# Kernel optimization log

Measured on AMD Instinct MI355X. Metric: run time of the kernel, lower is better.

## Reference

```python
import jax, jax.numpy as jnp
import numpy as np

N = 50000   # total nodes (50 graphs x 1000 nodes)
E = 800000  # edges (avg degree 16)
H = 128     # hidden_dim == input_dim
B = 50      # number of graphs
L = 3       # n_GNN_layers
NEG = 0.2   # LeakyReLU slope
EPS = 1e-5  # BatchNorm eps


def _lrelu(v):
    return jnp.where(v >= 0, v, NEG * v)


def setup_inputs() -> dict:
    key = jax.random.key(0)
    ks = jax.random.split(key, 16)
    s = 0.05
    inp = {
        "x": jax.random.normal(ks[0], (N, H), jnp.float32),
        "edge_index": jax.random.randint(ks[1], (2, E), 0, N, dtype=jnp.int64),
        "edge_attr": jax.random.uniform(ks[2], (E,), jnp.float32),
        "batch": jnp.sort(jax.random.randint(ks[3], (N,), 0, B, dtype=jnp.int64)),
        # per-layer GCN params (3 identical-shape layers stacked on axis 0)
        "Wg": (jax.random.normal(ks[4], (L, H, H)) * s).astype(jnp.float32),   # GCNConv.lin (no bias)
        "bg": jnp.zeros((L, H), jnp.float32),                                  # GCNConv.bias
        "We": (jax.random.normal(ks[5], (L, 2 * H, H)) * s).astype(jnp.float32),  # edge_lin
        "be": jnp.zeros((L, H), jnp.float32),
        "Wl": (jax.random.normal(ks[6], (L, H, H)) * s).astype(jnp.float32),   # post-conv Linear
        "bl": jnp.zeros((L, H), jnp.float32),
        "gamma": jnp.ones((L, H), jnp.float32),                                # BatchNorm affine
        "beta": jnp.zeros((L, H), jnp.float32),
        # final MLP head
        "Wf1": (jax.random.normal(ks[7], (H, H)) * s).astype(jnp.float32),
        "bf1": jnp.zeros((H,), jnp.float32),
        "Wf2": (jax.random.normal(ks[8], (H, H // 2)) * s).astype(jnp.float32),
        "bf2": jnp.zeros((H // 2,), jnp.float32),
        "Wf3": (jax.random.normal(ks[9], (H // 2, 2)) * s).astype(jnp.float32),
        "bf3": jnp.zeros((2,), jnp.float32),
    }
    return inp


def reference(x, edge_index, edge_attr, batch, Wg, bg, We, be, Wl, bl, gamma, beta,
              Wf1, bf1, Wf2, bf2, Wf3, bf3):
    n = x.shape[0]
    # edge_attr = |edge_attr| is used only for gcn_norm's edge weights, which the
    # 'node_concate' message ignores; self-loops from gcn_norm DO affect messages.
    _ = jnp.abs(edge_attr)
    loop = jnp.arange(n, dtype=edge_index.dtype)
    row = jnp.concatenate([edge_index[0], loop])  # source j
    col = jnp.concatenate([edge_index[1], loop])  # target i

    z = x
    for l in range(L):
        h = z @ Wg[l]                                           # GCNConv.lin (bias=False)
        msg = jnp.concatenate([h[col], h[row]], axis=1) @ We[l] + be[l]  # edge_lin(cat[x_i, x_j])
        agg = jax.ops.segment_sum(msg, col, num_segments=n) + bg[l]      # scatter-add + conv bias
        h2 = _lrelu(agg @ Wl[l] + bl[l])                        # Linear + LeakyReLU(0.2)
        mu = h2.mean(axis=0)
        var = h2.var(axis=0)                                    # biased var (BatchNorm training)
        z = gamma[l] * (h2 - mu) * jax.lax.rsqrt(var + EPS) + beta[l]

    # global_mean_pool over graph segments
    sums = jax.ops.segment_sum(z, batch, num_segments=B)
    cnt = jax.ops.segment_sum(jnp.ones((n, 1), z.dtype), batch, num_segments=B)
    pooled = sums / jnp.maximum(cnt, 1.0)

    h = _lrelu(pooled @ Wf1 + bf1)
    h = _lrelu(h @ Wf2 + bf2)
    return h @ Wf3 + bf3
```

## Files before the change

### kernel.cpp

```cpp
#include <hip/hip_runtime.h>
#include <hip/hip_fp16.h>

#define H 128
#define NEG 0.2f
#define EPSBN 1e-5f
#define BM 32

__device__ __forceinline__ float lrelu(float v){ return v >= 0.f ? v : NEG*v; }

union HU { __half2 h; unsigned int u; };

typedef __attribute__((ext_vector_type(8))) short bf16x8;
typedef __attribute__((ext_vector_type(4))) float f32x4;
#define MFMA16(a,b,c) __builtin_amdgcn_mfma_f32_16x16x32_bf16(a,b,c,0,0,0)

__device__ __forceinline__ unsigned short bf16_rn(float x){
  unsigned int u = __float_as_uint(x);
  u += 0x7fffu + ((u >> 16) & 1u);
  return (unsigned short)(u >> 16);
}
__device__ __forceinline__ float bf16f(unsigned short h){
  return __uint_as_float(((unsigned int)h) << 16);
}

__device__ __forceinline__ void asplit(const float* As, int aofs, bf16x8& ah, bf16x8& al){
  float av[8];
  *reinterpret_cast<float4*>(&av[0]) = *reinterpret_cast<const float4*>(&As[aofs]);
  *reinterpret_cast<float4*>(&av[4]) = *reinterpret_cast<const float4*>(&As[aofs+4]);
  #pragma unroll
  for (int j=0;j<8;j++){
    unsigned short h = bf16_rn(av[j]);
    ah[j] = (short)h;
    al[j] = (short)bf16_rn(av[j] - bf16f(h));
  }
}

__global__ void prep1_kernel(const float* __restrict__ We, const float* __restrict__ Wl,
                             float* __restrict__ Ntmp){
  int l = blockIdx.x >> 7;
  int k = blockIdx.x & 127;
  int j = threadIdx.x;
  __shared__ float WeS[2*H];
  if (j < H) WeS[j] = We[(size_t)(l*2*H + k)*H + j];
  else       WeS[j] = We[(size_t)(l*2*H + 128 + k)*H + (j-128)];
  __syncthreads();
  const float* wl = Wl + (size_t)l*H*H;
  int sel = (j >> 7) << 7;
  int jj = j & 127;
  float acc = 0.f;
  #pragma unroll 8
  for (int m=0;m<H;m++) acc += WeS[sel + m] * wl[m*H + jj];
  Ntmp[(size_t)(l*H + k)*256 + j] = acc;
}

__global__ void prep2_kernel(const float* __restrict__ Wg, const float* __restrict__ Ntmp,
                             float* __restrict__ Mcomb){
  int l = blockIdx.x >> 7;
  int k = blockIdx.x & 127;
  int j = threadIdx.x;
  __shared__ float WgS[H];
  if (j < H) WgS[j] = Wg[(size_t)(l*H + k)*H + j];
  __syncthreads();
  const float* nt = Ntmp + (size_t)l*H*256;
  float acc = 0.f;
  #pragma unroll 8
  for (int m=0;m<H;m++) acc += WgS[m] * nt[m*256 + j];
  Mcomb[(size_t)(l*H + k)*256 + j] = acc;
}

__global__ void prep3_kernel(const float* __restrict__ Mcomb,
                             unsigned short* __restrict__ Mfh, unsigned short* __restrict__ Mfl){
  int bid = blockIdx.x;
  int l  = bid >> 6;
  int ks = (bid >> 4) & 3;
  int ct = bid & 15;
  int lane = threadIdx.x;
  const float* M = Mcomb + (size_t)l*H*256;
  size_t base = ((((size_t)l*4 + ks)*16 + ct)*64 + lane)*8;
  int col = ct*16 + (lane & 15);
  int g = lane >> 4;
  #pragma unroll
  for (int j=0;j<8;j++){
    int k = ks*32 + 8*g + j;
    float v = M[(size_t)k*256 + col];
    unsigned short hi = bf16_rn(v);
    unsigned short lo = bf16_rn(v - bf16f(hi));
    Mfh[base + j] = hi;
    Mfl[base + j] = lo;
  }
}

__global__ void prepc_kernel(const float* __restrict__ be, const float* __restrict__ bg,
                             const float* __restrict__ bl, const float* __restrict__ Wl,
                             float* __restrict__ c1c2){
  int l = blockIdx.x;
  int j = threadIdx.x;
  const float* wl = Wl + (size_t)l*H*H;
  float a1=0.f, a2=0.f;
  for (int m=0;m<H;m++){ float w = wl[m*H + j]; a1 += be[l*H+m]*w; a2 += bg[l*H+m]*w; }
  c1c2[l*2*H + j]     = a1;
  c1c2[l*2*H + H + j] = a2 + bl[l*H + j];
}

__global__ void deg_kernel(const int* __restrict__ ei, int E, int* __restrict__ degI,
                           unsigned short* __restrict__ rankA){
  int e = blockIdx.x*blockDim.x + threadIdx.x;
  if (e < E){
    int r = atomicAdd(&degI[ei[E + e]], 1);
    rankA[e] = (unsigned short)r;
  }
}

__global__ void scan1_kernel(const int* __restrict__ degI, int n,
                             int* __restrict__ incl, int* __restrict__ bsum){
  int i = blockIdx.x*256 + threadIdx.x;
  __shared__ int sh[256];
  int v = (i < n) ? degI[i] : 0;
  sh[threadIdx.x] = v;
  __syncthreads();
  for (int ofs=1; ofs<256; ofs<<=1){
    int t = (threadIdx.x >= ofs) ? sh[threadIdx.x - ofs] : 0;
    __syncthreads();
    sh[threadIdx.x] += t;
    __syncthreads();
  }
  if (i < n) incl[i] = sh[threadIdx.x];
  if (threadIdx.x == 255) bsum[blockIdx.x] = sh[255];
}

__global__ void scan2_kernel(int* __restrict__ bsum, int nb){
  __shared__ int sh[256];
  int v = (threadIdx.x < nb) ? bsum[threadIdx.x] : 0;
  sh[threadIdx.x] = v;
  __syncthreads();
  for (int ofs=1; ofs<256; ofs<<=1){
    int t = (threadIdx.x >= ofs) ? sh[threadIdx.x - ofs] : 0;
    __syncthreads();
    sh[threadIdx.x] += t;
    __syncthreads();
  }
  if (threadIdx.x < nb) bsum[threadIdx.x] = sh[threadIdx.x] - v;
}

__global__ void scan3_kernel(const int* __restrict__ incl, const int* __restrict__ degI,
                             const int* __restrict__ bexcl, int n, int E,
                             int* __restrict__ rowptr){
  int i = blockIdx.x*256 + threadIdx.x;
  if (i < n){
    int start = incl[i] - degI[i] + bexcl[blockIdx.x];
    rowptr[i] = start;
    if (i == n-1) rowptr[n] = E;
  }
}

__global__ void fill_kernel(const int* __restrict__ ei, int E,
                            const int* __restrict__ rowptr, const unsigned short* __restrict__ rankA,
                            unsigned short* __restrict__ csr_src){
  int e = blockIdx.x*256 + threadIdx.x;
  if (e < E){
    int c = ei[E + e];
    int pos = rowptr[c] + (int)rankA[e];
    csr_src[pos] = (unsigned short)ei[e];
  }
}

__global__ void gofs_kernel(const int* __restrict__ batch, int n, int B, int* __restrict__ gofs){
  int i = blockIdx.x*256 + threadIdx.x;
  if (i >= n) return;
  if (i == 0){
    int b0 = batch[0];
    for (int g=0; g<=b0; g++) gofs[g] = 0;
  } else {
    int bp = batch[i-1], bc = batch[i];
    for (int g=bp+1; g<=bc; g++) gofs[g] = i;
  }
  if (i == n-1){
    int bl = batch[n-1];
    for (int g=bl+1; g<=B; g++) gofs[g] = n;
  }
}

#define KSBODY(KS, C, N, PREF) \
  { bf16x8 ah, al; asplit(As, arow_*132 + (KS)*32 + agrp, ah, al); \
    if (PREF){ int nb = fb + ((KS)+1)*1024; \
      N##U0h = Bh[nb];     N##U1h = Bh[nb+64];  N##U2h = Bh[nb+128]; N##U3h = Bh[nb+192]; \
      N##U0l = Bl[nb];     N##U1l = Bl[nb+64];  N##U2l = Bl[nb+128]; N##U3l = Bl[nb+192]; \
      N##V0h = Bh[nb+512]; N##V1h = Bh[nb+576]; N##V2h = Bh[nb+640]; N##V3h = Bh[nb+704]; } \
    accU[0]=MFMA16(ah,C##U0h,accU[0]); accU[0]=MFMA16(al,C##U0h,accU[0]); accU[0]=MFMA16(ah,C##U0l,accU[0]); \
    accV[0]=MFMA16(ah,C##V0h,accV[0]); accV[0]=MFMA16(al,C##V0h,accV[0]); \
    accU[1]=MFMA16(ah,C##U1h,accU[1]); accU[1]=MFMA16(al,C##U1h,accU[1]); accU[1]=MFMA16(ah,C##U1l,accU[1]); \
    accV[1]=MFMA16(ah,C##V1h,accV[1]); accV[1]=MFMA16(al,C##V1h,accV[1]); \
    accU[2]=MFMA16(ah,C##U2h,accU[2]); accU[2]=MFMA16(al,C##U2h,accU[2]); accU[2]=MFMA16(ah,C##U2l,accU[2]); \
    accV[2]=MFMA16(ah,C##V2h,accV[2]); accV[2]=MFMA16(al,C##V2h,accV[2]); \
    accU[3]=MFMA16(ah,C##U3h,accU[3]); accU[3]=MFMA16(al,C##U3h,accU[3]); accU[3]=MFMA16(ah,C##U3l,accU[3]); \
    accV[3]=MFMA16(ah,C##V3h,accV[3]); accV[3]=MFMA16(al,C##V3h,accV[3]); }

template<int XF>
__global__ __launch_bounds__(256)
void gemm_kernel(const float* __restrict__ Zin, const float* __restrict__ bnp,
                 const unsigned short* __restrict__ Mfh, const unsigned short* __restrict__ Mfl,
                 const float* __restrict__ c1c2, const int* __restrict__ degI,
                 int n, float* __restrict__ pre, __half* __restrict__ Vh){
  __shared__ float As[32*132];
  int brow = blockIdx.x * BM;
  int t = threadIdx.x;

  int lane = t & 63;
  int w = t >> 6;
  int rowtile = w & 1, colgroup = w >> 1;
  const bf16x8* Bh = reinterpret_cast<const bf16x8*>(Mfh);
  const bf16x8* Bl = reinterpret_cast<const bf16x8*>(Mfl);
  int fb = colgroup*4*64 + lane;

  bf16x8 cU0h,cU1h,cU2h,cU3h, cU0l,cU1l,cU2l,cU3l, cV0h,cV1h,cV2h,cV3h;
  bf16x8 nU0h,nU1h,nU2h,nU3h, nU0l,nU1l,nU2l,nU3l, nV0h,nV1h,nV2h,nV3h;
  cU0h = Bh[fb];     cU1h = Bh[fb+64];  cU2h = Bh[fb+128]; cU3h = Bh[fb+192];
  cU0l = Bl[fb];     cU1l = Bl[fb+64];  cU2l = Bl[fb+128]; cU3l = Bl[fb+192];
  cV0h = Bh[fb+512]; cV1h = Bh[fb+576]; cV2h = Bh[fb+640]; cV3h = Bh[fb+704];

  {
    int srow = t >> 3, sf = t & 7;
    int gr = brow + srow;
    bool act = (gr < n);
    const float* zrow = Zin + (size_t)gr*H;
    #pragma unroll
    for (int u=0; u<4; u++){
      int c4 = sf + 8*u;
      float4 g = make_float4(0.f,0.f,0.f,0.f);
      if (act) g = *reinterpret_cast<const float4*>(&zrow[c4*4]);
      if (XF){
        float4 sc4 = *reinterpret_cast<const float4*>(&bnp[c4*4]);
        float4 sh4 = *reinterpret_cast<const float4*>(&bnp[H + c4*4]);
        g.x = lrelu(g.x)*sc4.x + sh4.x;
        g.y = lrelu(g.y)*sc4.y + sh4.y;
        g.z = lrelu(g.z)*sc4.z + sh4.z;
        g.w = lrelu(g.w)*sc4.w + sh4.w;
      }
      *reinterpret_cast<float4*>(&As[srow*132 + c4*4]) = g;
    }
  }
  __syncthreads();

  f32x4 accU[4], accV[4];
  #pragma unroll
  for (int i=0;i<4;i++){
    accU[i] = (f32x4){0.f,0.f,0.f,0.f};
    accV[i] = (f32x4){0.f,0.f,0.f,0.f};
  }
  int arow_ = rowtile*16 + (lane & 15);
  int agrp  = (lane >> 4) << 3;

  KSBODY(0, c, n, 1)
  KSBODY(1, n, c, 1)
  KSBODY(2, c, n, 1)
  KSBODY(3, n, c, 0)

  int rowbase = brow + rowtile*16 + ((lane >> 4) << 2);
  float dg[4];
  #pragma unroll
  for (int r=0;r<4;r++){
    int gr = rowbase + r;
    dg[r] = (gr < n) ? (float)(degI[gr] + 1) : 0.f;
  }
  #pragma unroll
  for (int ctu=0; ctu<4; ctu++){
    int colU = colgroup*64 + ctu*16 + (lane & 15);
    float c1v = c1c2[colU], c2v = c1c2[H + colU];
    #pragma unroll
    for (int r=0;r<4;r++){
      int gr = rowbase + r;
      if (gr < n){
        float uu = accU[ctu][r], vv = accV[ctu][r];
        pre[(size_t)gr*H + colU] = dg[r]*(uu + c1v) + c2v + vv;
        Vh [(size_t)gr*H + colU] = __float2half(vv);
      }
    }
  }
}

__global__ __launch_bounds__(256)
void agg_kernel(const int* __restrict__ rowptr, const unsigned short* __restrict__ csr_src,
                const __half* __restrict__ Vh, float* __restrict__ pre, int n,
                float* __restrict__ partial){
  int node = blockIdx.x*8 + (threadIdx.x >> 5);
  int lane = threadIdx.x & 31;
  float4 h4 = make_float4(0.f,0.f,0.f,0.f);
  float4 q4 = make_float4(0.f,0.f,0.f,0.f);
  if (node < n){
    int p  = rowptr[node];
    int pe = rowptr[node+1];
    const __half* Vb = Vh + lane*4;
    float4 a = make_float4(0.f,0.f,0.f,0.f);
    for (; p+8 <= pe; p+=8){
      int s0 = csr_src[p],   s1 = csr_src[p+1], s2 = csr_src[p+2], s3 = csr_src[p+3];
      int s4 = csr_src[p+4], s5 = csr_src[p+5], s6 = csr_src[p+6], s7 = csr_src[p+7];
      uint2 r0 = *reinterpret_cast<const uint2*>(&Vb[(size_t)s0*H]);
      uint2 r1 = *reinterpret_cast<const uint2*>(&Vb[(size_t)s1*H]);
      uint2 r2 = *reinterpret_cast<const uint2*>(&Vb[(size_t)s2*H]);
      uint2 r3 = *reinterpret_cast<const uint2*>(&Vb[(size_t)s3*H]);
      uint2 r4 = *reinterpret_cast<const uint2*>(&Vb[(size_t)s4*H]);
      uint2 r5 = *reinterpret_cast<const uint2*>(&Vb[(size_t)s5*H]);
      uint2 r6 = *reinterpret_cast<const uint2*>(&Vb[(size_t)s6*H]);
      uint2 r7 = *reinterpret_cast<const uint2*>(&Vb[(size_t)s7*H]);
      HU ua, ub;
      float2 fa, fb;
      ua.u=r0.x; ub.u=r0.y; fa=__half22float2(ua.h); fb=__half22float2(ub.h);
      a.x+=fa.x; a.y+=fa.y; a.z+=fb.x; a.w+=fb.y;
      ua.u=r1.x; ub.u=r1.y; fa=__half22float2(ua.h); fb=__half22float2(ub.h);
      a.x+=fa.x; a.y+=fa.y; a.z+=fb.x; a.w+=fb.y;
      ua.u=r2.x; ub.u=r2.y; fa=__half22float2(ua.h); fb=__half22float2(ub.h);
      a.x+=fa.x; a.y+=fa.y; a.z+=fb.x; a.w+=fb.y;
      ua.u=r3.x; ub.u=r3.y; fa=__half22float2(ua.h); fb=__half22float2(ub.h);
      a.x+=fa.x; a.y+=fa.y; a.z+=fb.x; a.w+=fb.y;
      ua.u=r4.x; ub.u=r4.y; fa=__half22float2(ua.h); fb=__half22float2(ub.h);
      a.x+=fa.x; a.y+=fa.y; a.z+=fb.x; a.w+=fb.y;
      ua.u=r5.x; ub.u=r5.y; fa=__half22float2(ua.h); fb=__half22float2(ub.h);
      a.x+=fa.x; a.y+=fa.y; a.z+=fb.x; a.w+=fb.y;
      ua.u=r6.x; ub.u=r6.y; fa=__half22float2(ua.h); fb=__half22float2(ub.h);
      a.x+=fa.x; a.y+=fa.y; a.z+=fb.x; a.w+=fb.y;
      ua.u=r7.x; ub.u=r7.y; fa=__half22float2(ua.h); fb=__half22float2(ub.h);
      a.x+=fa.x; a.y+=fa.y; a.z+=fb.x; a.w+=fb.y;
    }
    for (; p+2 <= pe; p+=2){
      int s0 = csr_src[p], s1 = csr_src[p+1];
      uint2 r0 = *reinterpret_cast<const uint2*>(&Vb[(size_t)s0*H]);
      uint2 r1 = *reinterpret_cast<const uint2*>(&Vb[(size_t)s1*H]);
      HU ua, ub;
      float2 fa, fb;
      ua.u=r0.x; ub.u=r0.y; fa=__half22float2(ua.h); fb=__half22float2(ub.h);
      a.x+=fa.x; a.y+=fa.y; a.z+=fb.x; a.w+=fb.y;
      ua.u=r1.x; ub.u=r1.y; fa=__half22float2(ua.h); fb=__half22float2(ub.h);
      a.x+=fa.x; a.y+=fa.y; a.z+=fb.x; a.w+=fb.y;
    }
    for (; p < pe; p++){
      int s = csr_src[p];
      uint2 r = *reinterpret_cast<const uint2*>(&Vb[(size_t)s*H]);
      HU ua, ub; ua.u = r.x; ub.u = r.y;
      float2 fa = __half22float2(ua.h), fb = __half22float2(ub.h);
      a.x += fa.x; a.y += fa.y; a.z += fb.x; a.w += fb.y;
    }
    float4* pp = reinterpret_cast<float4*>(&pre[(size_t)node*H + lane*4]);
    float4 pr = *pp;
    pr.x += a.x; pr.y += a.y; pr.z += a.z; pr.w += a.w;
    *pp = pr;
    h4.x = lrelu(pr.x); h4.y = lrelu(pr.y); h4.z = lrelu(pr.z); h4.w = lrelu(pr.w);
    q4.x = h4.x*h4.x;   q4.y = h4.y*h4.y;   q4.z = h4.z*h4.z;   q4.w = h4.w*h4.w;
  }
  __shared__ float4 red[8][32];
  int slot = threadIdx.x >> 5;
  red[slot][lane] = h4;
  __syncthreads();
  if (threadIdx.x < 32){
    float4 tt = red[0][threadIdx.x];
    #pragma unroll
    for (int r=1;r<8;r++){
      float4 v = red[r][threadIdx.x];
      tt.x += v.x; tt.y += v.y; tt.z += v.z; tt.w += v.w;
    }
    *reinterpret_cast<float4*>(&partial[(size_t)blockIdx.x*256 + threadIdx.x*4]) = tt;
  }
  __syncthreads();
  red[slot][lane] = q4;
  __syncthreads();
  if (threadIdx.x < 32){
    float4 tt = red[0][threadIdx.x];
    #pragma unroll
    for (int r=1;r<8;r++){
      float4 v = red[r][threadIdx.x];
      tt.x += v.x; tt.y += v.y; tt.z += v.z; tt.w += v.w;
    }
    *reinterpret_cast<float4*>(&partial[(size_t)blockIdx.x*256 + 128 + threadIdx.x*4]) = tt;
  }
}

__global__ __launch_bounds__(256)
void redstats_kernel(const float* __restrict__ partial, int nb, float* __restrict__ bnsum,
                     const float* __restrict__ gamma, const float* __restrict__ beta,
                     float inv_n, float* __restrict__ scsh, int* __restrict__ cnt){
  int c = threadIdx.x;
  float acc = 0.f;
  for (int b = blockIdx.x; b < nb; b += 64)
    acc += partial[(size_t)b*256 + c];
  atomicAdd(&bnsum[c], acc);
  __threadfence();
  __shared__ int lastS;
  __syncthreads();
  if (threadIdx.x == 0){
    int prev = atomicAdd(cnt, 1);
    lastS = (prev == 63) ? 1 : 0;
  }
  __syncthreads();
  if (lastS && c < H){
    float s  = atomicAdd(&bnsum[c], 0.f);
    float ss = atomicAdd(&bnsum[H + c], 0.f);
    float mu  = s * inv_n;
    float var = ss * inv_n - mu*mu;
    float rs  = rsqrtf(fmaxf(var, 0.f) + EPSBN);
    float sc  = gamma[c] * rs;
    scsh[c]     = sc;
    scsh[H + c] = beta[c] - mu*sc;
  }
}

__global__ __launch_bounds__(256)
void pool_kernel(const float* __restrict__ pre, const float* __restrict__ scsh,
                 const int* __restrict__ gofs, float* __restrict__ pooled){
  int g    = blockIdx.x >> 3;
  int part = blockIdx.x & 7;
  int col  = threadIdx.x & 127;
  int half = threadIdx.x >> 7;
  int s = gofs[g], e = gofs[g+1];
  float sc = scsh[col], sh = scsh[H + col];
  float acc = 0.f;
  for (int r = s + part*2 + half; r < e; r += 16)
    acc += lrelu(pre[(size_t)r*H + col])*sc + sh;
  if (acc != 0.f || part == 0)
    atomicAdd(&pooled[(size_t)g*H + col], acc);
}

__global__ __launch_bounds__(128)
void head_kernel(const float* __restrict__ pooled, const int* __restrict__ gofs,
                 const float* __restrict__ Wf1, const float* __restrict__ bf1,
                 const float* __restrict__ Wf2, const float* __restrict__ bf2,
                 const float* __restrict__ Wf3, const float* __restrict__ bf3,
                 float* __restrict__ out){
  int g = blockIdx.x;
  int c = threadIdx.x;
  __shared__ float pm[128], h1[128], h2[64];
  float cf = fmaxf((float)(gofs[g+1] - gofs[g]), 1.f);
  pm[c] = pooled[(size_t)g*H + c] / cf;
  __syncthreads();
  float a = bf1[c];
  for (int k=0;k<H;k++) a += pm[k]*Wf1[k*H + c];
  h1[c] = lrelu(a);
  __syncthreads();
  if (c < 64){
    float b = bf2[c];
    for (int k=0;k<H;k++) b += h1[k]*Wf2[k*64 + c];
    h2[c] = lrelu(b);
  }
  __syncthreads();
  if (c < 2){
    float o = bf3[c];
    for (int k=0;k<64;k++) o += h2[k]*Wf3[k*2 + c];
    out[g*2 + c] = o;
  }
}

extern "C" void kernel_launch(void* const* d_in, const int* in_sizes, int n_in,
                              void* d_out, int out_size, void* d_ws, size_t ws_size,
                              hipStream_t stream){
  const float* x     = (const float*)d_in[0];
  const int*   ei    = (const int*)d_in[1];
  const int*   batch = (const int*)d_in[3];
  const float* Wg    = (const float*)d_in[4];
  const float* bg    = (const float*)d_in[5];
  const float* We    = (const float*)d_in[6];
  const float* be    = (const float*)d_in[7];
  const float* Wl    = (const float*)d_in[8];
  const float* bl    = (const float*)d_in[9];
  const float* gamma = (const float*)d_in[10];
  const float* beta  = (const float*)d_in[11];
  const float* Wf1   = (const float*)d_in[12];
  const float* bf1   = (const float*)d_in[13];
  const float* Wf2   = (const float*)d_in[14];
  const float* bf2   = (const float*)d_in[15];
  const float* Wf3   = (const float*)d_in[16];
  const float* bf3   = (const float*)d_in[17];
  float* out = (float*)d_out;

  int n = in_sizes[0] / H;
  int E = in_sizes[1] / 2;
  int B = out_size / 2;

  int nagg = (n + 7)/8;

  char* ws = (char*)d_ws;
  size_t off = 0;
  auto alloc = [&](size_t bytes)->void*{ void* p = ws + off; off += (bytes + 255) & ~255ULL; return p; };
  float*  pre    = (float*)alloc((size_t)n*H*4);
  __half* Vh     = (__half*)alloc((size_t)n*H*2);
  float*  Mcomb  = (float*)alloc((size_t)3*H*256*4);
  float*  Ntmp   = (float*)alloc((size_t)3*H*256*4);
  unsigned short* Mfh = (unsigned short*)alloc((size_t)3*4*16*64*8*2);
  unsigned short* Mfl = (unsigned short*)alloc((size_t)3*4*16*64*8*2);
  float*  c1c2   = (float*)alloc(3*2*H*4);
  float*  scsh   = (float*)alloc(3*2*H*4);
  int*    incl   = (int*)alloc((size_t)n*4);
  int*    bsum   = (int*)alloc(256*4);
  int*    rowptr = (int*)alloc((size_t)(n+1)*4);
  unsigned short* rankA   = (unsigned short*)alloc((size_t)E*2);
  unsigned short* csr_src = (unsigned short*)alloc((size_t)E*2);
  int*    gofs   = (int*)alloc((size_t)(B+1)*4);
  float*  partial= (float*)alloc((size_t)nagg*256*4);
  char* zbase = ws + off;
  float* bnsum  = (float*)alloc(3*2*H*4);
  int*   cnt    = (int*)alloc(3*4);
  int*   degI   = (int*)alloc((size_t)n*4);
  float* pooled = (float*)alloc((size_t)B*H*4);
  size_t zbytes = (size_t)((ws + off) - zbase);
  hipMemsetAsync(zbase, 0, zbytes, stream);

  prep1_kernel<<<3*H, 256, 0, stream>>>(We, Wl, Ntmp);
  prep2_kernel<<<3*H, 256, 0, stream>>>(Wg, Ntmp, Mcomb);
  prep3_kernel<<<3*64, 64, 0, stream>>>(Mcomb, Mfh, Mfl);
  prepc_kernel<<<3, 128, 0, stream>>>(be, bg, bl, Wl, c1c2);
  deg_kernel<<<(E+255)/256, 256, 0, stream>>>(ei, E, degI, rankA);

  int nb = (n + 255)/256;
  scan1_kernel<<<nb, 256, 0, stream>>>(degI, n, incl, bsum);
  scan2_kernel<<<1, 256, 0, stream>>>(bsum, nb);
  scan3_kernel<<<nb, 256, 0, stream>>>(incl, degI, bsum, n, E, rowptr);
  fill_kernel<<<(E+255)/256, 256, 0, stream>>>(ei, E, rowptr, rankA, csr_src);
  gofs_kernel<<<nb, 256, 0, stream>>>(batch, n, B, gofs);

  int gblocks = (n + BM - 1)/BM;
  size_t mstride = (size_t)4*16*64*8;
  for (int l=0; l<3; l++){
    if (l == 0)
      gemm_kernel<0><<<gblocks, 256, 0, stream>>>(x, nullptr, Mfh, Mfl, c1c2, degI, n, pre, Vh);
    else
      gemm_kernel<1><<<gblocks, 256, 0, stream>>>(pre, scsh + (l-1)*2*H, Mfh + l*mstride, Mfl + l*mstride,
                                                  c1c2 + l*2*H, degI, n, pre, Vh);
    agg_kernel<<<nagg, 256, 0, stream>>>(rowptr, csr_src, Vh, pre, n, partial);
    redstats_kernel<<<64, 256, 0, stream>>>(partial, nagg, bnsum + l*2*H,
                                            gamma + l*H, beta + l*H, 1.f/(float)n,
                                            scsh + l*2*H, cnt + l);
  }
  pool_kernel<<<B*8, 256, 0, stream>>>(pre, scsh + 2*2*H, gofs, pooled);
  head_kernel<<<B, 128, 0, stream>>>(pooled, gofs, Wf1, bf1, Wf2, bf2, Wf3, bf3, out);
}
```

Before: 397.0 us.

## Merge setup kernels into fewer launches and fuse pooling into last aggregation

Independent preprocessing kernels (weight folding, bias constants, degree counting, graph offsets, scans) are packed into three multi-role kernels, cutting the launch count. The final pool kernel is removed: the last aggregation pass accumulates post-LeakyReLU values per graph with atomics, and the head applies the BatchNorm scale/shift algebraically using node counts. It also skips writing back pre in the last layer. Risks include extra atomic contention and changed float summation order.

```diff
diff --git a/kernel.cpp b/kernel.cpp
--- a/kernel.cpp
+++ b/kernel.cpp
@@ -35,111 +35,137 @@
   }
 }
 
-__global__ void prep1_kernel(const float* __restrict__ We, const float* __restrict__ Wl,
-                             float* __restrict__ Ntmp){
-  int l = blockIdx.x >> 7;
-  int k = blockIdx.x & 127;
-  int j = threadIdx.x;
-  __shared__ float WeS[2*H];
-  if (j < H) WeS[j] = We[(size_t)(l*2*H + k)*H + j];
-  else       WeS[j] = We[(size_t)(l*2*H + 128 + k)*H + (j-128)];
-  __syncthreads();
-  const float* wl = Wl + (size_t)l*H*H;
-  int sel = (j >> 7) << 7;
-  int jj = j & 127;
-  float acc = 0.f;
-  #pragma unroll 8
-  for (int m=0;m<H;m++) acc += WeS[sel + m] * wl[m*H + jj];
-  Ntmp[(size_t)(l*H + k)*256 + j] = acc;
-}
-
-__global__ void prep2_kernel(const float* __restrict__ Wg, const float* __restrict__ Ntmp,
-                             float* __restrict__ Mcomb){
-  int l = blockIdx.x >> 7;
-  int k = blockIdx.x & 127;
-  int j = threadIdx.x;
-  __shared__ float WgS[H];
-  if (j < H) WgS[j] = Wg[(size_t)(l*H + k)*H + j];
-  __syncthreads();
-  const float* nt = Ntmp + (size_t)l*H*256;
-  float acc = 0.f;
-  #pragma unroll 8
-  for (int m=0;m<H;m++) acc += WgS[m] * nt[m*256 + j];
-  Mcomb[(size_t)(l*H + k)*256 + j] = acc;
-}
-
-__global__ void prep3_kernel(const float* __restrict__ Mcomb,
-                             unsigned short* __restrict__ Mfh, unsigned short* __restrict__ Mfl){
-  int bid = blockIdx.x;
-  int l  = bid >> 6;
-  int ks = (bid >> 4) & 3;
-  int ct = bid & 15;
-  int lane = threadIdx.x;
-  const float* M = Mcomb + (size_t)l*H*256;
-  size_t base = ((((size_t)l*4 + ks)*16 + ct)*64 + lane)*8;
-  int col = ct*16 + (lane & 15);
-  int g = lane >> 4;
-  #pragma unroll
-  for (int j=0;j<8;j++){
-    int k = ks*32 + 8*g + j;
-    float v = M[(size_t)k*256 + col];
-    unsigned short hi = bf16_rn(v);
-    unsigned short lo = bf16_rn(v - bf16f(hi));
-    Mfh[base + j] = hi;
-    Mfl[base + j] = lo;
-  }
-}
-
-__global__ void prepc_kernel(const float* __restrict__ be, const float* __restrict__ bg,
-                             const float* __restrict__ bl, const float* __restrict__ Wl,
-                             float* __restrict__ c1c2){
-  int l = blockIdx.x;
-  int j = threadIdx.x;
-  const float* wl = Wl + (size_t)l*H*H;
-  float a1=0.f, a2=0.f;
-  for (int m=0;m<H;m++){ float w = wl[m*H + j]; a1 += be[l*H+m]*w; a2 += bg[l*H+m]*w; }
-  c1c2[l*2*H + j]     = a1;
-  c1c2[l*2*H + H + j] = a2 + bl[l*H + j];
-}
-
-__global__ void deg_kernel(const int* __restrict__ ei, int E, int* __restrict__ degI,
-                           unsigned short* __restrict__ rankA){
-  int e = blockIdx.x*blockDim.x + threadIdx.x;
-  if (e < E){
-    int r = atomicAdd(&degI[ei[E + e]], 1);
-    rankA[e] = (unsigned short)r;
-  }
-}
-
-__global__ void scan1_kernel(const int* __restrict__ degI, int n,
-                             int* __restrict__ incl, int* __restrict__ bsum){
-  int i = blockIdx.x*256 + threadIdx.x;
-  __shared__ int sh[256];
-  int v = (i < n) ? degI[i] : 0;
-  sh[threadIdx.x] = v;
-  __syncthreads();
-  for (int ofs=1; ofs<256; ofs<<=1){
-    int t = (threadIdx.x >= ofs) ? sh[threadIdx.x - ofs] : 0;
+__global__ __launch_bounds__(256)
+void k1_kernel(const float* __restrict__ We, const float* __restrict__ Wl,
+               float* __restrict__ Ntmp,
+               const float* __restrict__ be, const float* __restrict__ bg,
+               const float* __restrict__ bl, float* __restrict__ c1c2,
+               const int* __restrict__ ei, int E, int* __restrict__ degI,
+               unsigned short* __restrict__ rankA,
+               const int* __restrict__ batch, int n, int B, int* __restrict__ gofs,
+               int nbDeg){
+  int b = blockIdx.x;
+  int t = threadIdx.x;
+  if (b < 3*H){
+    int l = b >> 7;
+    int k = b & 127;
+    __shared__ float WeS[2*H];
+    if (t < H) WeS[t] = We[(size_t)(l*2*H + k)*H + t];
+    else       WeS[t] = We[(size_t)(l*2*H + 128 + k)*H + (t-128)];
     __syncthreads();
-    sh[threadIdx.x] += t;
+    const float* wl = Wl + (size_t)l*H*H;
+    int sel = (t >> 7) << 7;
+    int jj = t & 127;
+    float acc = 0.f;
+    #pragma unroll 8
+    for (int m=0;m<H;m++) acc += WeS[sel + m] * wl[m*H + jj];
+    Ntmp[(size_t)(l*H + k)*256 + t] = acc;
+  } else if (b < 3*H + 3){
+    int l = b - 3*H;
+    if (t < H){
+      const float* wl = Wl + (size_t)l*H*H;
+      float a1=0.f, a2=0.f;
+      for (int m=0;m<H;m++){ float w = wl[m*H + t]; a1 += be[l*H+m]*w; a2 += bg[l*H+m]*w; }
+      c1c2[l*2*H + t]     = a1;
+      c1c2[l*2*H + H + t] = a2 + bl[l*H + t];
+    }
+  } else if (b < 3*H + 3 + nbDeg){
+    int e = (b - 3*H - 3)*256 + t;
+    if (e < E){
+      int r = atomicAdd(&degI[ei[E + e]], 1);
+      rankA[e] = (unsigned short)r;
+    }
+  } else {
+    int i = (b - 3*H - 3 - nbDeg)*256 + t;
+    if (i >= n) return;
+    if (i == 0){
+      int b0 = batch[0];
+      for (int g=0; g<=b0; g++) gofs[g] = 0;
+    } else {
+      int bp = batch[i-1], bc = batch[i];
+      for (int g=bp+1; g<=bc; g++) gofs[g] = i;
+    }
+    if (i == n-1){
+      int bl2 = batch[n-1];
+      for (int g=bl2+1; g<=B; g++) gofs[g] = n;
+    }
+  }
+}
+
+__global__ __launch_bounds__(256)
+void k2_kernel(const float* __restrict__ Wg, const float* __restrict__ Ntmp,
+               float* __restrict__ Mcomb,
+               const int* __restrict__ degI, int n,
+               int* __restrict__ incl, int* __restrict__ bsum){
+  int b = blockIdx.x;
+  int t = threadIdx.x;
+  if (b < 3*H){
+    int l = b >> 7;
+    int k = b & 127;
+    __shared__ float WgS[H];
+    if (t < H) WgS[t] = Wg[(size_t)(l*H + k)*H + t];
     __syncthreads();
-  }
-  if (i < n) incl[i] = sh[threadIdx.x];
-  if (threadIdx.x == 255) bsum[blockIdx.x] = sh[255];
-}
-
-__global__ void scan2_kernel(int* __restrict__ bsum, int nb){
-  __shared__ int sh[256];
-  int v = (threadIdx.x < nb) ? bsum[threadIdx.x] : 0;
-  sh[threadIdx.x] = v;
-  __syncthreads();
-  for (int ofs=1; ofs<256; ofs<<=1){
-    int t = (threadIdx.x >= ofs) ? sh[threadIdx.x - ofs] : 0;
+    const float* nt = Ntmp + (size_t)l*H*256;
+    float acc = 0.f;
+    #pragma unroll 8
+    for (int m=0;m<H;m++) acc += WgS[m] * nt[m*256 + t];
+    Mcomb[(size_t)(l*H + k)*256 + t] = acc;
+  } else {
+    int vb = b - 3*H;
+    int i = vb*256 + t;
+    __shared__ int sh[256];
+    int v = (i < n) ? degI[i] : 0;
+    sh[t] = v;
     __syncthreads();
-    sh[threadIdx.x] += t;
+    for (int ofs=1; ofs<256; ofs<<=1){
+      int tv = (t >= ofs) ? sh[t - ofs] : 0;
+      __syncthreads();
+      sh[t] += tv;
+      __syncthreads();
+    }
+    if (i < n) incl[i] = sh[t];
+    if (t == 255) bsum[vb] = sh[255];
+  }
+}
+
+__global__ __launch_bounds__(256)
+void k3_kernel(const float* __restrict__ Mcomb,
+               unsigned short* __restrict__ Mfh, unsigned short* __restrict__ Mfl,
+               int* __restrict__ bsum, int nb){
+  int b = blockIdx.x;
+  int t = threadIdx.x;
+  if (b < 3*64){
+    if (t >= 64) return;
+    int l  = b >> 6;
+    int ks = (b >> 4) & 3;
+    int ct = b & 15;
+    int lane = t;
+    const float* M = Mcomb + (size_t)l*H*256;
+    size_t base = ((((size_t)l*4 + ks)*16 + ct)*64 + lane)*8;
+    int col = ct*16 + (lane & 15);
+    int g = lane >> 4;
+    #pragma unroll
+    for (int j=0;j<8;j++){
+      int k = ks*32 + 8*g + j;
+      float v = M[(size_t)k*256 + col];
+      unsigned short hi = bf16_rn(v);
+      unsigned short lo = bf16_rn(v - bf16f(hi));
+      Mfh[base + j] = hi;
+      Mfl[base + j] = lo;
+    }
+  } else {
+    __shared__ int sh[256];
+    int v = (t < nb) ? bsum[t] : 0;
+    sh[t] = v;
     __syncthreads();
-  }
-  if (threadIdx.x < nb) bsum[threadIdx.x] = sh[threadIdx.x] - v;
+    for (int ofs=1; ofs<256; ofs<<=1){
+      int tv = (t >= ofs) ? sh[t - ofs] : 0;
+      __syncthreads();
+      sh[t] += tv;
+      __syncthreads();
+    }
+    if (t < nb) bsum[t] = sh[t] - v;
+  }
 }
 
 __global__ void scan3_kernel(const int* __restrict__ incl, const int* __restrict__ degI,
@@ -161,22 +187,6 @@
     int c = ei[E + e];
     int pos = rowptr[c] + (int)rankA[e];
     csr_src[pos] = (unsigned short)ei[e];
-  }
-}
-
-__global__ void gofs_kernel(const int* __restrict__ batch, int n, int B, int* __restrict__ gofs){
-  int i = blockIdx.x*256 + threadIdx.x;
-  if (i >= n) return;
-  if (i == 0){
-    int b0 = batch[0];
-    for (int g=0; g<=b0; g++) gofs[g] = 0;
-  } else {
-    int bp = batch[i-1], bc = batch[i];
-    for (int g=bp+1; g<=bc; g++) gofs[g] = i;
-  }
-  if (i == n-1){
-    int bl = batch[n-1];
-    for (int g=bl+1; g<=B; g++) gofs[g] = n;
   }
 }
 
@@ -278,10 +288,12 @@
   }
 }
 
+template<int LAST>
 __global__ __launch_bounds__(256)
 void agg_kernel(const int* __restrict__ rowptr, const unsigned short* __restrict__ csr_src,
                 const __half* __restrict__ Vh, float* __restrict__ pre, int n,
-                float* __restrict__ partial){
+                float* __restrict__ partial,
+                const int* __restrict__ batch, float* __restrict__ pooled){
   int node = blockIdx.x*8 + (threadIdx.x >> 5);
   int lane = threadIdx.x & 31;
   float4 h4 = make_float4(0.f,0.f,0.f,0.f);
@@ -342,13 +354,20 @@
     float4* pp = reinterpret_cast<float4*>(&pre[(size_t)node*H + lane*4]);
     float4 pr = *pp;
     pr.x += a.x; pr.y += a.y; pr.z += a.z; pr.w += a.w;
-    *pp = pr;
+    if (!LAST) *pp = pr;
     h4.x = lrelu(pr.x); h4.y = lrelu(pr.y); h4.z = lrelu(pr.z); h4.w = lrelu(pr.w);
     q4.x = h4.x*h4.x;   q4.y = h4.y*h4.y;   q4.z = h4.z*h4.z;   q4.w = h4.w*h4.w;
   }
   __shared__ float4 red[8][32];
+  __shared__ int gsh[2];
   int slot = threadIdx.x >> 5;
   red[slot][lane] = h4;
+  if (LAST && threadIdx.x == 0){
+    int n0 = blockIdx.x*8;
+    int n7 = n0 + 7; if (n7 >= n) n7 = n - 1;
+    gsh[0] = batch[n0 < n ? n0 : n-1];
+    gsh[1] = batch[n7];
+  }
   __syncthreads();
   if (threadIdx.x < 32){
     float4 tt = red[0][threadIdx.x];
@@ -358,6 +377,17 @@
       tt.x += v.x; tt.y += v.y; tt.z += v.z; tt.w += v.w;
     }
     *reinterpret_cast<float4*>(&partial[(size_t)blockIdx.x*256 + threadIdx.x*4]) = tt;
+    if (LAST && gsh[0] == gsh[1]){
+      float* pp2 = &pooled[(size_t)gsh[0]*H + threadIdx.x*4];
+      atomicAdd(pp2+0, tt.x); atomicAdd(pp2+1, tt.y);
+      atomicAdd(pp2+2, tt.z); atomicAdd(pp2+3, tt.w);
+    }
+  }
+  if (LAST && gsh[0] != gsh[1] && node < n){
+    int g = batch[node];
+    float* pp2 = &pooled[(size_t)g*H + lane*4];
+    atomicAdd(pp2+0, h4.x); atomicAdd(pp2+1, h4.y);
+    atomicAdd(pp2+2, h4.z); atomicAdd(pp2+3, h4.w);
   }
   __syncthreads();
   red[slot][lane] = q4;
@@ -402,24 +432,9 @@
   }
 }
 
-__global__ __launch_bounds__(256)
-void pool_kernel(const float* __restrict__ pre, const float* __restrict__ scsh,
-                 const int* __restrict__ gofs, float* __restrict__ pooled){
-  int g    = blockIdx.x >> 3;
-  int part = blockIdx.x & 7;
-  int col  = threadIdx.x & 127;
-  int half = threadIdx.x >> 7;
-  int s = gofs[g], e = gofs[g+1];
-  float sc = scsh[col], sh = scsh[H + col];
-  float acc = 0.f;
-  for (int r = s + part*2 + half; r < e; r += 16)
-    acc += lrelu(pre[(size_t)r*H + col])*sc + sh;
-  if (acc != 0.f || part == 0)
-    atomicAdd(&pooled[(size_t)g*H + col], acc);
-}
-
 __global__ __launch_bounds__(128)
-void head_kernel(const float* __restrict__ pooled, const int* __restrict__ gofs,
+void head_kernel(const float* __restrict__ pooled, const float* __restrict__ scsh,
+                 const int* __restrict__ gofs,
                  const float* __restrict__ Wf1, const float* __restrict__ bf1,
                  const float* __restrict__ Wf2, const float* __restrict__ bf2,
                  const float* __restrict__ Wf3, const float* __restrict__ bf3,
@@ -427,8 +442,9 @@
   int g = blockIdx.x;
   int c = threadIdx.x;
   __shared__ float pm[128], h1[128], h2[64];
-  float cf = fmaxf((float)(gofs[g+1] - gofs[g]), 1.f);
-  pm[c] = pooled[(size_t)g*H + c] / cf;
+  float cntf = (float)(gofs[g+1] - gofs[g]);
+  float cf = fmaxf(cntf, 1.f);
+  pm[c] = (scsh[c]*pooled[(size_t)g*H + c] + scsh[H + c]*cntf) / cf;
   __syncthreads();
   float a = bf1[c];
   for (int k=0;k<H;k++) a += pm[k]*Wf1[k*H + c];
@@ -474,6 +490,8 @@
   int B = out_size / 2;
 
   int nagg = (n + 7)/8;
+  int nb   = (n + 255)/256;
+  int nbDeg = (E + 255)/256;
 
   char* ws = (char*)d_ws;
   size_t off = 0;
@@ -501,18 +519,12 @@
   size_t zbytes = (size_t)((ws + off) - zbase);
   hipMemsetAsync(zbase, 0, zbytes, stream);
 
-  prep1_kernel<<<3*H, 256, 0, stream>>>(We, Wl, Ntmp);
-  prep2_kernel<<<3*H, 256, 0, stream>>>(Wg, Ntmp, Mcomb);
-  prep3_kernel<<<3*64, 64, 0, stream>>>(Mcomb, Mfh, Mfl);
-  prepc_kernel<<<3, 128, 0, stream>>>(be, bg, bl, Wl, c1c2);
-  deg_kernel<<<(E+255)/256, 256, 0, stream>>>(ei, E, degI, rankA);
-
-  int nb = (n + 255)/256;
-  scan1_kernel<<<nb, 256, 0, stream>>>(degI, n, incl, bsum);
-  scan2_kernel<<<1, 256, 0, stream>>>(bsum, nb);
+  k1_kernel<<<3*H + 3 + nbDeg + nb, 256, 0, stream>>>(We, Wl, Ntmp, be, bg, bl, c1c2,
+                                                      ei, E, degI, rankA, batch, n, B, gofs, nbDeg);
+  k2_kernel<<<3*H + nb, 256, 0, stream>>>(Wg, Ntmp, Mcomb, degI, n, incl, bsum);
+  k3_kernel<<<3*64 + 1, 256, 0, stream>>>(Mcomb, Mfh, Mfl, bsum, nb);
   scan3_kernel<<<nb, 256, 0, stream>>>(incl, degI, bsum, n, E, rowptr);
-  fill_kernel<<<(E+255)/256, 256, 0, stream>>>(ei, E, rowptr, rankA, csr_src);
-  gofs_kernel<<<nb, 256, 0, stream>>>(batch, n, B, gofs);
+  fill_kernel<<<nbDeg, 256, 0, stream>>>(ei, E, rowptr, rankA, csr_src);
 
   int gblocks = (n + BM - 1)/BM;
   size_t mstride = (size_t)4*16*64*8;
@@ -522,11 +534,13 @@
     else
       gemm_kernel<1><<<gblocks, 256, 0, stream>>>(pre, scsh + (l-1)*2*H, Mfh + l*mstride, Mfl + l*mstride,
                                                   c1c2 + l*2*H, degI, n, pre, Vh);
-    agg_kernel<<<nagg, 256, 0, stream>>>(rowptr, csr_src, Vh, pre, n, partial);
+    if (l < 2)
+      agg_kernel<0><<<nagg, 256, 0, stream>>>(rowptr, csr_src, Vh, pre, n, partial, nullptr, nullptr);
+    else
+      agg_kernel<1><<<nagg, 256, 0, stream>>>(rowptr, csr_src, Vh, pre, n, partial, batch, pooled);
     redstats_kernel<<<64, 256, 0, stream>>>(partial, nagg, bnsum + l*2*H,
                                             gamma + l*H, beta + l*H, 1.f/(float)n,
                                             scsh + l*2*H, cnt + l);
   }
-  pool_kernel<<<B*8, 256, 0, stream>>>(pre, scsh + 2*2*H, gofs, pooled);
-  head_kernel<<<B, 128, 0, stream>>>(pooled, gofs, Wf1, bf1, Wf2, bf2, Wf3, bf3, out);
-}
+  head_kernel<<<B, 128, 0, stream>>>(pooled, scsh + 2*2*H, gofs, Wf1, bf1, Wf2, bf2, Wf3, bf3, out);
+}
```

Measured after the change: 391.4 us. Within noise of the previous version (-1.4%).
